# Kernel optimization log

Measured on AMD Instinct MI355X. Metric: run time of the kernel, lower is better.

Reference implementation:

```python
import jax, jax.numpy as jnp
import numpy as np

NUM_CLASSES = 80
IOU_EPS = 1e-5


def _corners(b):
    # NormalizeBoxes with default shape=ones((2,)) divides by 1 -> plain corner transform
    cx, cy, w, h = b[..., 0], b[..., 1], b[..., 2], b[..., 3]
    return cy - h / 2, cx - w / 2, cy + h / 2, cx + w / 2  # y1, x1, y2, x2


def _pairwise_iou(gt, pr):
    # gt: [B,G,4], pr: [P,4] -> [B,G,P]
    ga = gt[..., 2] * gt[..., 3]                      # [B,G]
    pa = pr[:, 2] * pr[:, 3]                          # [P]
    gy1, gx1, gy2, gx2 = _corners(gt)                 # [B,G]
    py1, px1, py2, px2 = _corners(pr)                 # [P]
    ih = jnp.maximum(0.0, jnp.minimum(gy2[..., None], py2) - jnp.maximum(gy1[..., None], py1))
    iw = jnp.maximum(0.0, jnp.minimum(gx2[..., None], px2) - jnp.maximum(gx1[..., None], px1))
    inter = iw * ih
    union = ga[..., None] + pa - inter
    return inter / (union + IOU_EPS)


def _assign_boxes(gt_boxes, pr_boxes):
    B, G, _ = gt_boxes.shape
    P = pr_boxes.shape[1]
    gt_labels = gt_boxes[..., -2]                     # [B,G]
    gt_conf = gt_boxes[..., -1]                       # [B,G]
    pr = pr_boxes[0].astype(jnp.float32)              # priors shared across batch: [P,4]

    iou = _pairwise_iou(gt_boxes[..., :4].astype(jnp.float32), pr)  # [B,G,P]
    valid = (gt_boxes[..., 0] != -1.0).astype(iou.dtype)
    iou = iou * valid[..., None]

    # matches: all pairs with iou>=0.5, plus the argmax prior per valid (conf>0) GT.
    thresh = iou >= 0.5                                             # [B,G,P]
    best_p = jnp.argmax(iou, axis=-1)                               # [B,G]
    best = (jnp.arange(P)[None, None, :] == best_p[..., None]) & (gt_conf > 0.0)[..., None]

    # thresh matches then best matches -> best overrides thresh; within each
    g_ids = jnp.arange(G)[None, :, None]
    g_thresh = jnp.max(jnp.where(thresh, g_ids, -1), axis=1)        # [B,P]
    g_best = jnp.max(jnp.where(best, g_ids, -1), axis=1)            # [B,P]
    win_g = jnp.where(g_best >= 0, g_best, g_thresh)                # [B,P]
    matched = win_g >= 0

    labels = jnp.take_along_axis(gt_labels, jnp.maximum(win_g, 0), axis=1)  # [B,P]
    cls_id = jnp.where(matched, labels.astype(jnp.int32), NUM_CLASSES)
    onehot = jax.nn.one_hot(cls_id, NUM_CLASSES + 1, dtype=jnp.float32)     # [B,P,C+1]
    assign_mask = onehot[..., -1]                                           # 1 = background
    ignore = jnp.any((iou < 0.5) & (iou >= 0.4), axis=1)                    # [B,P]
    assign_mask = jnp.where(ignore, -1.0, assign_mask)

    # loc targets: tf.scatter_nd SUMS duplicate indices, so each (b,p) target is the
    # sum of encodings over all its matches (thresh + best, duplicates counted twice).
    w = thresh.astype(jnp.float32) + best.astype(jnp.float32)       # [B,G,P]
    gb = gt_boxes[..., :4].astype(jnp.float32)
    safe_log = lambda v: jnp.where(v > 0, jnp.log(jnp.maximum(v, 1e-20)), 0.0)
    W = jnp.sum(w, axis=1)                                          # [B,P] match counts
    S_cx = jnp.einsum('bgp,bg->bp', w, gb[..., 0])
    S_cy = jnp.einsum('bgp,bg->bp', w, gb[..., 1])
    S_lw = jnp.einsum('bgp,bg->bp', w, safe_log(gb[..., 2]))
    S_lh = jnp.einsum('bgp,bg->bp', w, safe_log(gb[..., 3]))
    p_cx, p_cy, p_w, p_h = pr[:, 0], pr[:, 1], pr[:, 2], pr[:, 3]   # [P]
    hat_cx = (S_cx - W * p_cx) / p_w
    hat_cy = (S_cy - W * p_cy) / p_h
    hat_w = S_lw - W * jnp.log(p_w)
    hat_h = S_lh - W * jnp.log(p_h)
    loc_true = jnp.stack([hat_cx, hat_cy, hat_w, hat_h], axis=2)    # [B,P,4]

    cls_true = onehot[..., :NUM_CLASSES]
    return cls_true, loc_true, assign_mask[..., None]


def setup_inputs() -> dict:
    key = jax.random.key(0)
    ks = jax.random.split(key, 8)
    B, G, P = 8, 64, 32768
    NUM_VALID = 48
    g_cx = jax.random.uniform(ks[0], (B, G), minval=0.05, maxval=0.95)
    g_cy = jax.random.uniform(ks[1], (B, G), minval=0.05, maxval=0.95)
    g_w = jax.random.uniform(ks[2], (B, G), minval=0.02, maxval=0.30)
    g_h = jax.random.uniform(ks[3], (B, G), minval=0.02, maxval=0.30)
    labels = jax.random.randint(ks[4], (B, G), 0, NUM_CLASSES).astype(jnp.float32)
    conf = jnp.ones((B, G), dtype=jnp.float32)
    gt = jnp.stack([g_cx, g_cy, g_w, g_h, labels, conf], axis=-1)
    valid = (jnp.arange(G) < NUM_VALID)[None, :, None]
    gt_boxes = jnp.where(valid, gt, -1.0)  # pad trailing GTs with -1 (conf -1 <= 0)
    p_cx = jax.random.uniform(ks[5], (P,), minval=0.0, maxval=1.0)
    p_cy = jax.random.uniform(ks[6], (P,), minval=0.0, maxval=1.0)
    pwh = jax.random.uniform(ks[7], (P, 2), minval=0.02, maxval=0.30)
    pr = jnp.concatenate([p_cx[:, None], p_cy[:, None], pwh], axis=1)
    pr_boxes = jnp.broadcast_to(pr[None], (B, P, 4))
    return {"gt_boxes": gt_boxes, "pr_boxes": pr_boxes}


def reference(gt_boxes, pr_boxes):
    return _assign_boxes(gt_boxes, pr_boxes)
```

## Files before the change

kernel.cpp:

```cpp
#include <hip/hip_runtime.h>
#include <cmath>

#define NBATCH 8
#define NGT    64
#define NPR    32768
#define NC     80

#define CHUNKS 16
#define CHUNK  (NPR / CHUNKS)
#define GTPB   8

__global__ __launch_bounds__(256) void k_bestp_part(const float* __restrict__ gt,
                                                    const float* __restrict__ pr,
                                                    float* __restrict__ pval,
                                                    int* __restrict__ pidx) {
#pragma clang fp contract(off)
    const int chunk = blockIdx.x;
    const int gg    = blockIdx.y;
    const int tid   = threadIdx.x;

    __shared__ float sy1[GTPB], sx1[GTPB], sy2[GTPB], sx2[GTPB], sga[GTPB];
    __shared__ int   sv[GTPB];
    if (tid < GTPB) {
        const float* g6 = gt + ((size_t)gg * GTPB + tid) * 6;
        float cx = g6[0], cy = g6[1], w = g6[2], h = g6[3];
        sy1[tid] = cy - h * 0.5f;
        sx1[tid] = cx - w * 0.5f;
        sy2[tid] = cy + h * 0.5f;
        sx2[tid] = cx + w * 0.5f;
        sga[tid] = w * h;
        sv[tid]  = (cx != -1.0f) ? 1 : 0;
    }
    __syncthreads();

    float gy1[GTPB], gx1[GTPB], gy2[GTPB], gx2[GTPB], ga[GTPB];
    int   gv[GTPB];
    #pragma unroll
    for (int j = 0; j < GTPB; ++j) {
        gy1[j] = sy1[j]; gx1[j] = sx1[j]; gy2[j] = sy2[j]; gx2[j] = sx2[j];
        ga[j] = sga[j]; gv[j] = sv[j];
    }

    float best[GTPB]; int bi[GTPB];
    #pragma unroll
    for (int j = 0; j < GTPB; ++j) { best[j] = -1.0f; bi[j] = 0; }

    const int base = chunk * CHUNK;
    #pragma unroll 4
    for (int k = 0; k < CHUNK / 256; ++k) {
        int p = base + k * 256 + tid;
        float4 pv = ((const float4*)pr)[p];
        float py1 = pv.y - pv.w * 0.5f;
        float px1 = pv.x - pv.z * 0.5f;
        float py2 = pv.y + pv.w * 0.5f;
        float px2 = pv.x + pv.z * 0.5f;
        float pa  = pv.z * pv.w;
        #pragma unroll
        for (int j = 0; j < GTPB; ++j) {
            float ih = fmaxf(0.0f, fminf(gy2[j], py2) - fmaxf(gy1[j], py1));
            float iw = fmaxf(0.0f, fminf(gx2[j], px2) - fmaxf(gx1[j], px1));
            float inter = iw * ih;
            float uni   = ga[j] + pa - inter;
            float iou   = inter / (uni + 1e-5f);
            iou = gv[j] ? iou : 0.0f;
            if (iou > best[j]) { best[j] = iou; bi[j] = p; }
        }
    }

    #pragma unroll
    for (int j = 0; j < GTPB; ++j) {
        #pragma unroll
        for (int off = 32; off > 0; off >>= 1) {
            float ov = __shfl_down(best[j], off);
            int   oi = __shfl_down(bi[j], off);
            if (ov > best[j] || (ov == best[j] && oi < bi[j])) {
                best[j] = ov; bi[j] = oi;
            }
        }
    }

    __shared__ float rv[4][GTPB];
    __shared__ int   rix[4][GTPB];
    const int wave = tid >> 6;
    if ((tid & 63) == 0) {
        #pragma unroll
        for (int j = 0; j < GTPB; ++j) { rv[wave][j] = best[j]; rix[wave][j] = bi[j]; }
    }
    __syncthreads();
    if (tid < GTPB) {
        float v = rv[0][tid]; int i = rix[0][tid];
        #pragma unroll
        for (int w = 1; w < 4; ++w) {
            float v2 = rv[w][tid]; int i2 = rix[w][tid];
            if (v2 > v || (v2 == v && i2 < i)) { v = v2; i = i2; }
        }
        int bg = gg * GTPB + tid;
        pval[bg * CHUNKS + chunk] = v;
        pidx[bg * CHUNKS + chunk] = i;
    }
}

__global__ __launch_bounds__(256) void k_assign(const float* __restrict__ gt,
                                                const float* __restrict__ pr,
                                                const float* __restrict__ pval,
                                                const int* __restrict__ pidx,
                                                float* __restrict__ out_cls,
                                                float* __restrict__ out_loc,
                                                float* __restrict__ out_msk) {
#pragma clang fp contract(off)
    const int b   = blockIdx.y;
    const int tid = threadIdx.x;
    const int p   = blockIdx.x * 256 + tid;

    __shared__ float s_cx[NGT], s_cy[NGT], s_y1[NGT], s_x1[NGT], s_y2[NGT], s_x2[NGT];
    __shared__ float s_ga[NGT], s_lw[NGT], s_lh[NGT], s_lab[NGT], s_conf[NGT];
    __shared__ int   s_bp[NGT], s_val[NGT];
    __shared__ int   s_cls[256];

    if (tid < NGT) {
        const float* g6 = gt + ((size_t)b * NGT + tid) * 6;
        float cx = g6[0], cy = g6[1], w = g6[2], h = g6[3];
        s_cx[tid] = cx; s_cy[tid] = cy;
        s_y1[tid] = cy - h * 0.5f;
        s_x1[tid] = cx - w * 0.5f;
        s_y2[tid] = cy + h * 0.5f;
        s_x2[tid] = cx + w * 0.5f;
        s_ga[tid] = w * h;
        s_lw[tid] = (w > 0.0f) ? logf(fmaxf(w, 1e-20f)) : 0.0f;
        s_lh[tid] = (h > 0.0f) ? logf(fmaxf(h, 1e-20f)) : 0.0f;
        s_lab[tid]  = g6[4];
        s_conf[tid] = g6[5];
        s_val[tid]  = (cx != -1.0f) ? 1 : 0;
        int bg = b * NGT + tid;
        float v = pval[bg * CHUNKS + 0]; int i = pidx[bg * CHUNKS + 0];
        #pragma unroll
        for (int c = 1; c < CHUNKS; ++c) {
            float v2 = pval[bg * CHUNKS + c]; int i2 = pidx[bg * CHUNKS + c];
            if (v2 > v || (v2 == v && i2 < i)) { v = v2; i = i2; }
        }
        s_bp[tid] = i;
    }
    __syncthreads();

    float4 pv = ((const float4*)pr)[p];
    const float px = pv.x, py = pv.y, pw = pv.z, ph = pv.w;
    const float py1 = py - ph * 0.5f;
    const float px1 = px - pw * 0.5f;
    const float py2 = py + ph * 0.5f;
    const float px2 = px + pw * 0.5f;
    const float pa  = pw * ph;

    int  g_th = -1, g_bs = -1;
    bool ignore = false;
    float W = 0.0f, Scx = 0.0f, Scy = 0.0f, Slw = 0.0f, Slh = 0.0f;

    for (int g = 0; g < NGT; ++g) {
        float ih = fmaxf(0.0f, fminf(s_y2[g], py2) - fmaxf(s_y1[g], py1));
        float iw = fmaxf(0.0f, fminf(s_x2[g], px2) - fmaxf(s_x1[g], px1));
        float inter = iw * ih;
        float uni   = s_ga[g] + pa - inter;
        float iou   = inter / (uni + 1e-5f);
        iou = s_val[g] ? iou : 0.0f;
        bool th = (iou >= 0.5f);
        bool bs = (s_bp[g] == p) && (s_conf[g] > 0.0f);
        if (th) g_th = g;
        if (bs) g_bs = g;
        ignore = ignore || (iou < 0.5f && iou >= 0.4f);
        float wg = (float)th + (float)bs;
        W   += wg;
        Scx += wg * s_cx[g];
        Scy += wg * s_cy[g];
        Slw += wg * s_lw[g];
        Slh += wg * s_lh[g];
    }

    const int  win     = (g_bs >= 0) ? g_bs : g_th;
    const bool matched = (win >= 0);
    const int  cls     = matched ? (int)s_lab[win] : NC;
    float msk = matched ? 0.0f : 1.0f;
    if (ignore) msk = -1.0f;

    const float hcx = (Scx - W * px) / pw;
    const float hcy = (Scy - W * py) / ph;
    const float hw  = Slw - W * logf(pw);
    const float hh  = Slh - W * logf(ph);

    const size_t bp_i = (size_t)b * NPR + p;
    ((float4*)out_loc)[bp_i] = make_float4(hcx, hcy, hw, hh);
    out_msk[bp_i] = msk;

    s_cls[tid] = cls;
    __syncthreads();
    const size_t base4 = ((size_t)b * NPR + (size_t)blockIdx.x * 256) * NC / 4;
    float4* oc4 = (float4*)out_cls;
    #pragma unroll
    for (int k = 0; k < (256 * NC / 4) / 256; ++k) {
        int idx = tid + k * 256;
        int e0  = idx * 4;
        int pl  = e0 / NC;
        int c0  = e0 - pl * NC;
        int cl  = s_cls[pl];
        float4 v;
        v.x = (c0     == cl) ? 1.0f : 0.0f;
        v.y = (c0 + 1 == cl) ? 1.0f : 0.0f;
        v.z = (c0 + 2 == cl) ? 1.0f : 0.0f;
        v.w = (c0 + 3 == cl) ? 1.0f : 0.0f;
        oc4[base4 + idx] = v;
    }
}

extern "C" void kernel_launch(void* const* d_in, const int* in_sizes, int n_in,
                              void* d_out, int out_size, void* d_ws, size_t ws_size,
                              hipStream_t stream) {
    const float* gt = (const float*)d_in[0];
    const float* pr = (const float*)d_in[1];

    float* pval = (float*)d_ws;
    int*   pidx = (int*)((char*)d_ws + NBATCH * NGT * CHUNKS * sizeof(float));

    float* out_cls = (float*)d_out;
    float* out_loc = out_cls + (size_t)NBATCH * NPR * NC;
    float* out_msk = out_loc + (size_t)NBATCH * NPR * 4;

    dim3 g1(CHUNKS, NBATCH * NGT / GTPB);
    k_bestp_part<<<g1, 256, 0, stream>>>(gt, pr, pval, pidx);

    dim3 g2(NPR / 256, NBATCH);
    k_assign<<<g2, 256, 0, stream>>>(gt, pr, pval, pidx, out_cls, out_loc, out_msk);
}
```

Before: 134.1 us.

## Precompute per-GT parameters in a separate kernel and read via uniform float4 loads

Adds a small k_finish kernel that reduces the chunked argmax results once per GT and packs corners, area, centers, label, log sizes and the best-prior index into three float4s per GT. k_assign no longer does the redundant per-block GT setup, 16-way reduction, shared-memory fill and first barrier; it reads the packed data with wave-uniform float4 loads, likely scalar loads, in an unrolled loop. Invalid GTs get a huge y1/y2 so IoU is zero without a validity select, and conf>0 is folded into the stored index. The cost is an extra kernel launch and a dependence on cached global loads in place of LDS.

Result: no change. 135.7 us (+1.2%).

```diff
diff --git a/kernel.cpp b/kernel.cpp
--- a/kernel.cpp
+++ b/kernel.cpp
@@ -100,10 +100,41 @@
     }
 }
 
-__global__ __launch_bounds__(256) void k_assign(const float* __restrict__ gt,
-                                                const float* __restrict__ pr,
+__global__ __launch_bounds__(256) void k_finish(const float* __restrict__ gt,
                                                 const float* __restrict__ pval,
                                                 const int* __restrict__ pidx,
+                                                float* __restrict__ prep) {
+#pragma clang fp contract(off)
+    const int bg = blockIdx.x * 256 + threadIdx.x;
+    if (bg >= NBATCH * NGT) return;
+    const float* g6 = gt + (size_t)bg * 6;
+    float cx = g6[0], cy = g6[1], w = g6[2], h = g6[3], lab = g6[4], conf = g6[5];
+    bool valid = (cx != -1.0f);
+    float y1 = cy - h * 0.5f;
+    float x1 = cx - w * 0.5f;
+    float y2 = cy + h * 0.5f;
+    float x2 = cx + w * 0.5f;
+    if (!valid) { y1 = 3e38f; y2 = 3e38f; }
+    float ga = w * h;
+    float lw = (w > 0.0f) ? logf(fmaxf(w, 1e-20f)) : 0.0f;
+    float lh = (h > 0.0f) ? logf(fmaxf(h, 1e-20f)) : 0.0f;
+
+    float v = pval[bg * CHUNKS + 0]; int i = pidx[bg * CHUNKS + 0];
+    #pragma unroll
+    for (int c = 1; c < CHUNKS; ++c) {
+        float v2 = pval[bg * CHUNKS + c]; int i2 = pidx[bg * CHUNKS + c];
+        if (v2 > v || (v2 == v && i2 < i)) { v = v2; i = i2; }
+    }
+    int bp = (conf > 0.0f) ? i : -1;
+
+    float4* q = (float4*)prep + (size_t)bg * 3;
+    q[0] = make_float4(y1, x1, y2, x2);
+    q[1] = make_float4(ga, cx, cy, lab);
+    q[2] = make_float4(lw, lh, __int_as_float(bp), 0.0f);
+}
+
+__global__ __launch_bounds__(256) void k_assign(const float* __restrict__ pr,
+                                                const float* __restrict__ prep,
                                                 float* __restrict__ out_cls,
                                                 float* __restrict__ out_loc,
                                                 float* __restrict__ out_msk) {
@@ -112,35 +143,7 @@
     const int tid = threadIdx.x;
     const int p   = blockIdx.x * 256 + tid;
 
-    __shared__ float s_cx[NGT], s_cy[NGT], s_y1[NGT], s_x1[NGT], s_y2[NGT], s_x2[NGT];
-    __shared__ float s_ga[NGT], s_lw[NGT], s_lh[NGT], s_lab[NGT], s_conf[NGT];
-    __shared__ int   s_bp[NGT], s_val[NGT];
-    __shared__ int   s_cls[256];
-
-    if (tid < NGT) {
-        const float* g6 = gt + ((size_t)b * NGT + tid) * 6;
-        float cx = g6[0], cy = g6[1], w = g6[2], h = g6[3];
-        s_cx[tid] = cx; s_cy[tid] = cy;
-        s_y1[tid] = cy - h * 0.5f;
-        s_x1[tid] = cx - w * 0.5f;
-        s_y2[tid] = cy + h * 0.5f;
-        s_x2[tid] = cx + w * 0.5f;
-        s_ga[tid] = w * h;
-        s_lw[tid] = (w > 0.0f) ? logf(fmaxf(w, 1e-20f)) : 0.0f;
-        s_lh[tid] = (h > 0.0f) ? logf(fmaxf(h, 1e-20f)) : 0.0f;
-        s_lab[tid]  = g6[4];
-        s_conf[tid] = g6[5];
-        s_val[tid]  = (cx != -1.0f) ? 1 : 0;
-        int bg = b * NGT + tid;
-        float v = pval[bg * CHUNKS + 0]; int i = pidx[bg * CHUNKS + 0];
-        #pragma unroll
-        for (int c = 1; c < CHUNKS; ++c) {
-            float v2 = pval[bg * CHUNKS + c]; int i2 = pidx[bg * CHUNKS + c];
-            if (v2 > v || (v2 == v && i2 < i)) { v = v2; i = i2; }
-        }
-        s_bp[tid] = i;
-    }
-    __syncthreads();
+    const float4* __restrict__ q = (const float4*)prep + (size_t)b * NGT * 3;
 
     float4 pv = ((const float4*)pr)[p];
     const float px = pv.x, py = pv.y, pw = pv.z, ph = pv.w;
@@ -154,29 +157,33 @@
     bool ignore = false;
     float W = 0.0f, Scx = 0.0f, Scy = 0.0f, Slw = 0.0f, Slh = 0.0f;
 
+    #pragma unroll 8
     for (int g = 0; g < NGT; ++g) {
-        float ih = fmaxf(0.0f, fminf(s_y2[g], py2) - fmaxf(s_y1[g], py1));
-        float iw = fmaxf(0.0f, fminf(s_x2[g], px2) - fmaxf(s_x1[g], px1));
+        float4 q0 = q[3 * g + 0];
+        float4 q1 = q[3 * g + 1];
+        float4 q2 = q[3 * g + 2];
+        float ih = fmaxf(0.0f, fminf(q0.z, py2) - fmaxf(q0.x, py1));
+        float iw = fmaxf(0.0f, fminf(q0.w, px2) - fmaxf(q0.y, px1));
         float inter = iw * ih;
-        float uni   = s_ga[g] + pa - inter;
+        float uni   = q1.x + pa - inter;
         float iou   = inter / (uni + 1e-5f);
-        iou = s_val[g] ? iou : 0.0f;
         bool th = (iou >= 0.5f);
-        bool bs = (s_bp[g] == p) && (s_conf[g] > 0.0f);
+        bool bs = (__float_as_int(q2.z) == p);
         if (th) g_th = g;
         if (bs) g_bs = g;
         ignore = ignore || (iou < 0.5f && iou >= 0.4f);
         float wg = (float)th + (float)bs;
         W   += wg;
-        Scx += wg * s_cx[g];
-        Scy += wg * s_cy[g];
-        Slw += wg * s_lw[g];
-        Slh += wg * s_lh[g];
+        Scx += wg * q1.y;
+        Scy += wg * q1.z;
+        Slw += wg * q2.x;
+        Slh += wg * q2.y;
     }
 
     const int  win     = (g_bs >= 0) ? g_bs : g_th;
     const bool matched = (win >= 0);
-    const int  cls     = matched ? (int)s_lab[win] : NC;
+    float labf = prep[((size_t)b * NGT + (win >= 0 ? win : 0)) * 12 + 7];
+    const int cls = matched ? (int)labf : NC;
     float msk = matched ? 0.0f : 1.0f;
     if (ignore) msk = -1.0f;
 
@@ -189,6 +196,7 @@
     ((float4*)out_loc)[bp_i] = make_float4(hcx, hcy, hw, hh);
     out_msk[bp_i] = msk;
 
+    __shared__ int s_cls[256];
     s_cls[tid] = cls;
     __syncthreads();
     const size_t base4 = ((size_t)b * NPR + (size_t)blockIdx.x * 256) * NC / 4;
@@ -216,7 +224,8 @@
     const float* pr = (const float*)d_in[1];
 
     float* pval = (float*)d_ws;
-    int*   pidx = (int*)((char*)d_ws + NBATCH * NGT * CHUNKS * sizeof(float));
+    int*   pidx = (int*)((char*)d_ws + 32 * 1024);
+    float* prep = (float*)((char*)d_ws + 64 * 1024);
 
     float* out_cls = (float*)d_out;
     float* out_loc = out_cls + (size_t)NBATCH * NPR * NC;
@@ -225,6 +234,8 @@
     dim3 g1(CHUNKS, NBATCH * NGT / GTPB);
     k_bestp_part<<<g1, 256, 0, stream>>>(gt, pr, pval, pidx);
 
+    k_finish<<<(NBATCH * NGT + 255) / 256, 256, 0, stream>>>(gt, pval, pidx, prep);
+
     dim3 g2(NPR / 256, NBATCH);
-    k_assign<<<g2, 256, 0, stream>>>(gt, pr, pval, pidx, out_cls, out_loc, out_msk);
-}
+    k_assign<<<g2, 256, 0, stream>>>(pr, prep, out_cls, out_loc, out_msk);
+}
```
